# Performance work log

Hardware: AMD Instinct MI355X
Metric: run time of the kernel (lower is better)

Reference implementation:

```python
import jax, jax.numpy as jnp
import numpy as np

N_NODES = 80000
N_EDGES = 1280000
IN_CH = 128
HID = 64
N_GRAPHS = 64
DROPOUT_P = 0.3


def setup_inputs() -> dict:
    key = jax.random.key(0)
    ks = jax.random.split(key, 12)
    x = jax.random.normal(ks[0], (N_NODES, IN_CH), dtype=jnp.float32)
    edge_index = jax.random.randint(ks[1], (2, N_EDGES), 0, N_NODES, dtype=jnp.int64 if jax.config.read('jax_enable_x64') else jnp.int32)
    batch = jnp.sort(jax.random.randint(ks[2], (N_NODES,), 0, N_GRAPHS))
    def lin(k, fan_in, fan_out):
        lim = 1.0 / np.sqrt(fan_in)
        kw, kb = jax.random.split(k)
        W = jax.random.uniform(kw, (fan_in, fan_out), minval=-lim, maxval=lim, dtype=jnp.float32)
        b = jax.random.uniform(kb, (fan_out,), minval=-lim, maxval=lim, dtype=jnp.float32)
        return W, b
    W1, b1 = lin(ks[3], IN_CH, HID)
    W2, b2 = lin(ks[4], HID, HID)
    W3, b3 = lin(ks[5], HID, HID)
    Wm1, bm1 = lin(ks[6], HID, HID)
    Wm2, bm2 = lin(ks[7], HID, 1)
    return {"x": x, "edge_index": edge_index, "batch": batch,
            "W1": W1, "b1": b1, "W2": W2, "b2": b2, "W3": W3, "b3": b3,
            "Wm1": Wm1, "bm1": bm1, "Wm2": Wm2, "bm2": bm2}


def _gcn_conv(x, W, b, src, dst, deg_inv_sqrt):
    # PyG GCNConv: h = X W; add self-loops; norm_e = d^-1/2[src] * d^-1/2[dst]
    h = x @ W  # [N, F]
    norm = deg_inv_sqrt[src] * deg_inv_sqrt[dst]  # [E]
    agg = jax.ops.segment_sum(h[src] * norm[:, None], dst, num_segments=x.shape[0])
    agg = agg + h * (deg_inv_sqrt * deg_inv_sqrt)[:, None]  # self-loop term d^-1
    return agg + b


def _dropout(x, key, p):
    keep = jax.random.bernoulli(key, 1.0 - p, x.shape)
    return jnp.where(keep, x / (1.0 - p), 0.0)


def reference(x, edge_index, batch, W1, b1, W2, b2, W3, b3, Wm1, bm1, Wm2, bm2):
    src, dst = edge_index[0], edge_index[1]
    N = x.shape[0]
    # in-degree on dst, +1 for self-loop (PyG default normalization)
    deg = jax.ops.segment_sum(jnp.ones_like(dst, dtype=x.dtype), dst, num_segments=N) + 1.0
    deg_inv_sqrt = jax.lax.rsqrt(deg)

    dk = jax.random.split(jax.random.key(42), 4)
    h = _dropout(jax.nn.relu(_gcn_conv(x, W1, b1, src, dst, deg_inv_sqrt)), dk[0], DROPOUT_P)
    h = _dropout(jax.nn.relu(_gcn_conv(h, W2, b2, src, dst, deg_inv_sqrt)), dk[1], DROPOUT_P)
    h = _dropout(jax.nn.relu(_gcn_conv(h, W3, b3, src, dst, deg_inv_sqrt)), dk[2], DROPOUT_P)

    # global mean pool per graph
    sums = jax.ops.segment_sum(h, batch, num_segments=N_GRAPHS)
    counts = jax.ops.segment_sum(jnp.ones((N,), dtype=h.dtype), batch, num_segments=N_GRAPHS)
    pooled = sums / jnp.maximum(counts, 1.0)[:, None]  # [G, HID]

    # MLP head: Linear -> ReLU -> Dropout -> Linear
    m = jax.nn.relu(pooled @ Wm1 + bm1)
    m = _dropout(m, dk[3], DROPOUT_P)
    return m @ Wm2 + bm2  # [G, 1]
```

## Files before the change

kernel.cpp:

```cpp
#include <hip/hip_runtime.h>
#include <hip/hip_fp8.h>
#include <stdint.h>

#define HID 64
#define INCH 128
#define NGRAPH 64
#define KEEPP 0.7f
#define CAP 64
#define CAPSH 6
#define BD 16

typedef __attribute__((ext_vector_type(8))) short short8;
typedef __attribute__((ext_vector_type(4))) float floatx4;

__device__ __forceinline__ uint8_t f2e4(float f) {
  __hip_fp8_e4m3 t(f);
  return (uint8_t)t.__x;
}
__device__ __forceinline__ float e42f(uint8_t b) {
  __hip_fp8_e4m3 t;
  t.__x = (__hip_fp8_storage_t)b;
  return (float)t;
}
__device__ __forceinline__ ushort f2bf(float v) {
  uint32_t u = __float_as_uint(v);
  return (ushort)((u + 0x7FFFu + ((u >> 16) & 1u)) >> 16);
}
__device__ __forceinline__ float bf2f(ushort b) {
  return __uint_as_float((uint32_t)b << 16);
}

__host__ __device__ inline void tf2x32(uint32_t k0, uint32_t k1,
                                       uint32_t& x0, uint32_t& x1) {
  const uint32_t ks2 = k0 ^ k1 ^ 0x1BD11BDAu;
#define ROTL32(v, d) (((v) << (d)) | ((v) >> (32 - (d))))
#define TF_RND(r) { x0 += x1; x1 = ROTL32(x1, r); x1 ^= x0; }
  x0 += k0; x1 += k1;
  TF_RND(13) TF_RND(15) TF_RND(26) TF_RND(6)
  x0 += k1;  x1 += ks2 + 1u;
  TF_RND(17) TF_RND(29) TF_RND(16) TF_RND(24)
  x0 += ks2; x1 += k0 + 2u;
  TF_RND(13) TF_RND(15) TF_RND(26) TF_RND(6)
  x0 += k0;  x1 += k1 + 3u;
  TF_RND(17) TF_RND(29) TF_RND(16) TF_RND(24)
  x0 += k1;  x1 += ks2 + 4u;
  TF_RND(13) TF_RND(15) TF_RND(26) TF_RND(6)
  x0 += ks2; x1 += k0 + 5u;
#undef TF_RND
#undef ROTL32
}

__device__ __forceinline__ bool keep_mask(uint32_t k0, uint32_t k1, uint32_t idx) {
  uint32_t x0 = 0u, x1 = idx;
  tf2x32(k0, k1, x0, x1);
  uint32_t bits = x0 ^ x1;
  float u = __uint_as_float((bits >> 9) | 0x3f800000u) - 1.0f;
  return u < KEEPP;
}

__device__ __forceinline__ void wsplit_one(const float* __restrict__ W,
                                           short8* __restrict__ Wh,
                                           short8* __restrict__ Wl, int i) {
  int lane = i & 63, f = i >> 6;
  int kc = f >> 2, ct = f & 3;
  int kbase = kc * 32 + ((lane >> 4) << 3);
  int n = ct * 16 + (lane & 15);
  short8 h, l;
#pragma unroll
  for (int j = 0; j < 8; ++j) {
    float w = W[(size_t)(kbase + j) * HID + n];
    uint32_t u = __float_as_uint(w);
    h[j] = (short)(u >> 16);
    float r = w - __uint_as_float(u & 0xFFFF0000u);
    l[j] = (short)(__float_as_uint(r) >> 16);
  }
  Wh[i] = h;
  Wl[i] = l;
}

__global__ __launch_bounds__(256) void k_w1(const float* __restrict__ W1,
                                            short8* __restrict__ Wh1,
                                            short8* __restrict__ Wl1) {
  wsplit_one(W1, Wh1, Wl1, blockIdx.x * 256 + (int)threadIdx.x);
}

template <int K>
__device__ __forceinline__ void mgemm_tile_f32(const float* __restrict__ A,
                                               const short8* __restrict__ Wh,
                                               const short8* __restrict__ Wl,
                                               ushort* __restrict__ C,
                                               int N, int tile) {
  constexpr int KC = K / 32;
  const int lane = threadIdx.x & 63;
  const int wv = threadIdx.x >> 6;
  const int m = lane & 15;
  const int q = lane >> 4;
  const int row0 = tile * 64 + wv * 16;
  if (row0 >= N) return;
  const int arow = min(row0 + m, N - 1);
  const float* __restrict__ ap = A + (size_t)arow * K + (q << 3);

  floatx4 acc[4];
#pragma unroll
  for (int ct = 0; ct < 4; ++ct) acc[ct] = (floatx4){0.f, 0.f, 0.f, 0.f};

#pragma unroll
  for (int kc = 0; kc < KC; ++kc) {
    const floatx4* apv = (const floatx4*)(ap + kc * 32);
    floatx4 x0 = apv[0];
    floatx4 x1 = apv[1];
    short8 ah, al;
#pragma unroll
    for (int j = 0; j < 4; ++j) {
      uint32_t u = __float_as_uint(x0[j]);
      ah[j] = (short)(u >> 16);
      float r = x0[j] - __uint_as_float(u & 0xFFFF0000u);
      al[j] = (short)(__float_as_uint(r) >> 16);
    }
#pragma unroll
    for (int j = 0; j < 4; ++j) {
      uint32_t u = __float_as_uint(x1[j]);
      ah[4 + j] = (short)(u >> 16);
      float r = x1[j] - __uint_as_float(u & 0xFFFF0000u);
      al[4 + j] = (short)(__float_as_uint(r) >> 16);
    }
#pragma unroll
    for (int ct = 0; ct < 4; ++ct) {
      short8 bh = Wh[(kc * 4 + ct) * 64 + lane];
      short8 bl = Wl[(kc * 4 + ct) * 64 + lane];
      acc[ct] = __builtin_amdgcn_mfma_f32_16x16x32_bf16(ah, bh, acc[ct], 0, 0, 0);
      acc[ct] = __builtin_amdgcn_mfma_f32_16x16x32_bf16(ah, bl, acc[ct], 0, 0, 0);
      acc[ct] = __builtin_amdgcn_mfma_f32_16x16x32_bf16(al, bh, acc[ct], 0, 0, 0);
    }
  }

  ushort* __restrict__ cp = C + (size_t)row0 * HID;
#pragma unroll
  for (int ct = 0; ct < 4; ++ct)
#pragma unroll
    for (int r = 0; r < 4; ++r) {
      int rr = (q << 2) + r;
      if (row0 + rr < N) cp[(size_t)rr * HID + ct * 16 + m] = f2bf(acc[ct][r]);
    }
}

template <int K>
__global__ __launch_bounds__(256) void k_build_gemm(
    const float* __restrict__ A, const short8* __restrict__ Wh,
    const short8* __restrict__ Wl, ushort* __restrict__ C, int N,
    const int* __restrict__ src, const int* __restrict__ dst,
    int* __restrict__ counts, int* __restrict__ cap,
    int E, int build_blocks, int gemm_blocks,
    const float* __restrict__ W2, short8* __restrict__ Wh2, short8* __restrict__ Wl2,
    const float* __restrict__ W3, short8* __restrict__ Wh3, short8* __restrict__ Wl3,
    const int* __restrict__ batch, int* __restrict__ gends) {
  const int TB = build_blocks + gemm_blocks;
  const int tid = (int)threadIdx.x;
  if ((int)blockIdx.x >= TB) {
    int xb = (int)blockIdx.x - TB;
    if (xb < 2) {
      wsplit_one(W2, Wh2, Wl2, xb * 256 + tid);
    } else if (xb < 4) {
      wsplit_one(W3, Wh3, Wl3, (xb - 2) * 256 + tid);
    } else {
      int bi = xb - 4;
      for (int i = bi * 256 + tid; i < N; i += BD * 256) {
        int g = batch[i];
        int gn = (i + 1 < N) ? batch[i + 1] : -1;
        if (g != gn) gends[g] = i + 1;
      }
    }
    return;
  }
  const long T = (long)TB;
  const long b = (long)blockIdx.x;
  const long gb = (b * gemm_blocks) / T;
  const bool is_g = (((b + 1) * gemm_blocks) / T) != gb;
  if (!is_g) {
    int bb = (int)(b - gb);
    int e = bb * 256 + tid;
    if (e < E) {
      int s = src[e], d = dst[e];
      int r = atomicAdd(&counts[d], 1);
      if (r < CAP) cap[(d << CAPSH) + r] = s;
    }
    return;
  }
  mgemm_tile_f32<K>(A, Wh, Wl, C, N, (int)gb);
}

template <int K>
__global__ __launch_bounds__(256) void k_mgemm_b(const ushort* __restrict__ A,
                                                 const short8* __restrict__ Wh,
                                                 const short8* __restrict__ Wl,
                                                 uint8_t* __restrict__ C,
                                                 const int* __restrict__ counts,
                                                 int N) {
  constexpr int KC = K / 32;
  const int lane = threadIdx.x & 63;
  const int wv = threadIdx.x >> 6;
  const int m = lane & 15;
  const int q = lane >> 4;
  const int row0 = (int)blockIdx.x * 64 + wv * 16;
  if (row0 >= N) return;
  const int arow = min(row0 + m, N - 1);
  const ushort* __restrict__ ap = A + (size_t)arow * K + (q << 3);

  floatx4 acc[4];
#pragma unroll
  for (int ct = 0; ct < 4; ++ct) acc[ct] = (floatx4){0.f, 0.f, 0.f, 0.f};

#pragma unroll
  for (int kc = 0; kc < KC; ++kc) {
    short8 ah = *(const short8*)(ap + kc * 32);
#pragma unroll
    for (int ct = 0; ct < 4; ++ct) {
      short8 bh = Wh[(kc * 4 + ct) * 64 + lane];
      short8 bl = Wl[(kc * 4 + ct) * 64 + lane];
      acc[ct] = __builtin_amdgcn_mfma_f32_16x16x32_bf16(ah, bh, acc[ct], 0, 0, 0);
      acc[ct] = __builtin_amdgcn_mfma_f32_16x16x32_bf16(ah, bl, acc[ct], 0, 0, 0);
    }
  }

  float dv[4];
#pragma unroll
  for (int r = 0; r < 4; ++r) {
    int gr = min(row0 + (q << 2) + r, N - 1);
    dv[r] = rsqrtf((float)counts[gr] + 1.0f);
  }
  uint8_t* __restrict__ cp = C + (size_t)row0 * HID;
#pragma unroll
  for (int ct = 0; ct < 4; ++ct)
#pragma unroll
    for (int r = 0; r < 4; ++r) {
      int rr = (q << 2) + r;
      if (row0 + rr < N) cp[(size_t)rr * HID + ct * 16 + m] = f2e4(acc[ct][r] * dv[r]);
    }
}

__global__ __launch_bounds__(256) void k_scale(const ushort* __restrict__ Bh,
                                               const int* __restrict__ counts,
                                               uint8_t* __restrict__ B0, int N) {
  int t = blockIdx.x * 256 + threadIdx.x;
  int total = N * (HID / 8);
  if (t >= total) return;
  int node = t >> 3;
  float dn = rsqrtf((float)counts[node] + 1.0f);
  const ushort* ip = Bh + (size_t)t * 8;
  ushort4 a = *(const ushort4*)ip;
  ushort4 b = *(const ushort4*)(ip + 4);
  uint8_t o[8];
  o[0] = f2e4(bf2f(a.x) * dn); o[1] = f2e4(bf2f(a.y) * dn);
  o[2] = f2e4(bf2f(a.z) * dn); o[3] = f2e4(bf2f(a.w) * dn);
  o[4] = f2e4(bf2f(b.x) * dn); o[5] = f2e4(bf2f(b.y) * dn);
  o[6] = f2e4(bf2f(b.z) * dn); o[7] = f2e4(bf2f(b.w) * dn);
  *(uint2*)(B0 + (size_t)t * 8) = *(uint2*)o;
}

__global__ __launch_bounds__(256) void k_gather_s(const uint8_t* __restrict__ tmp,
                                                  const int* __restrict__ counts,
                                                  const int* __restrict__ cap,
                                                  const float* __restrict__ bias,
                                                  ushort* __restrict__ outh, int N,
                                                  uint32_t k0, uint32_t k1) {
  const int node = blockIdx.x * 4 + (threadIdx.x >> 6);
  const int lane = threadIdx.x & 63;
  if (node >= N) return;
  const int degn = __builtin_amdgcn_readfirstlane(counts[node]);
  const int deg = min(degn, CAP);
  const int base = node << CAPSH;
  const int idx = node * HID + lane;
  const float selfv = e42f(tmp[idx]);
  const float blane = bias[lane];
  const int sub = lane >> 4;
  const int ch4 = (lane & 15) << 2;
  float a0 = 0.0f, a1 = 0.0f, a2 = 0.0f, a3 = 0.0f;
  for (int j = 0; j < deg; j += 8) {
    int4 ea = *(const int4*)&cap[base + j];
    int4 eb = *(const int4*)&cap[base + j + 4];
    int sa = (sub & 1) ? ea.y : ea.x;
    int ta = (sub & 1) ? ea.w : ea.z;
    sa = (sub & 2) ? ta : sa;
    int sb = (sub & 1) ? eb.y : eb.x;
    int tb = (sub & 1) ? eb.w : eb.z;
    sb = (sub & 2) ? tb : sb;
    uint32_t wa = 0u, wb = 0u;
    if (j + sub < deg)
      wa = *(const uint32_t*)(tmp + ((size_t)sa << 6) + ch4);
    if (j + 4 + sub < deg)
      wb = *(const uint32_t*)(tmp + ((size_t)sb << 6) + ch4);
    a0 += e42f((uint8_t)(wa & 255u));
    a1 += e42f((uint8_t)((wa >> 8) & 255u));
    a2 += e42f((uint8_t)((wa >> 16) & 255u));
    a3 += e42f((uint8_t)(wa >> 24));
    a0 += e42f((uint8_t)(wb & 255u));
    a1 += e42f((uint8_t)((wb >> 8) & 255u));
    a2 += e42f((uint8_t)((wb >> 16) & 255u));
    a3 += e42f((uint8_t)(wb >> 24));
  }
  a0 += __shfl_xor(a0, 16); a1 += __shfl_xor(a1, 16);
  a2 += __shfl_xor(a2, 16); a3 += __shfl_xor(a3, 16);
  a0 += __shfl_xor(a0, 32); a1 += __shfl_xor(a1, 32);
  a2 += __shfl_xor(a2, 32); a3 += __shfl_xor(a3, 32);
  const int srcl = lane >> 2;
  float t0 = __shfl(a0, srcl);
  float t1 = __shfl(a1, srcl);
  float t2 = __shfl(a2, srcl);
  float t3 = __shfl(a3, srcl);
  float u01 = (lane & 1) ? t1 : t0;
  float u23 = (lane & 1) ? t3 : t2;
  float acc = (lane & 2) ? u23 : u01;

  const float dn = rsqrtf((float)degn + 1.0f);
  float v = dn * (acc + selfv) + blane;
  v = fmaxf(v, 0.0f);
  v = keep_mask(k0, k1, (uint32_t)idx) ? v / KEEPP : 0.0f;
  outh[idx] = f2bf(v);
}

__global__ __launch_bounds__(256) void k_pool(const ushort* __restrict__ h,
                                              const int* __restrict__ batch,
                                              float* __restrict__ sums, int N) {
  __shared__ float ls[NGRAPH * HID];
  for (int i = threadIdx.x; i < NGRAPH * HID; i += 256) ls[i] = 0.0f;
  __syncthreads();
  const int lane = threadIdx.x & 63;
  const int wave = threadIdx.x >> 6;
  int per = (N + gridDim.x - 1) / gridDim.x;
  int beg = blockIdx.x * per;
  int end = min(N, beg + per);
  for (int i = beg + wave; i < end; i += 4) {
    int g = batch[i];
    atomicAdd(&ls[g * HID + lane], bf2f(h[(size_t)i * HID + lane]));
  }
  __syncthreads();
  for (int i = threadIdx.x; i < NGRAPH * HID; i += 256)
    if (ls[i] != 0.0f) atomicAdd(&sums[i], ls[i]);
}

__global__ __launch_bounds__(256) void k_head(const float* __restrict__ sums,
                                              const int* __restrict__ gends,
                                              const float* __restrict__ Wm1,
                                              const float* __restrict__ bm1,
                                              const float* __restrict__ Wm2,
                                              const float* __restrict__ bm2,
                                              float* __restrict__ out,
                                              uint32_t k0, uint32_t k1) {
  __shared__ float cnts_s[NGRAPH];
  __shared__ float pooled[NGRAPH * HID];
  __shared__ float m[NGRAPH * HID];
  if (threadIdx.x < 64) {
    int g = threadIdx.x;
    int e = gends[g];
#pragma unroll
    for (int off = 1; off < 64; off <<= 1) {
      int o = __shfl_up(e, off);
      if (g >= off) e = max(e, o);
    }
    int prev = __shfl_up(e, 1);
    if (g == 0) prev = 0;
    cnts_s[g] = (float)(e - prev);
  }
  __syncthreads();
  for (int i = threadIdx.x; i < NGRAPH * HID; i += 256) {
    int g = i >> 6;
    pooled[i] = sums[i] / fmaxf(cnts_s[g], 1.0f);
  }
  __syncthreads();
  for (int i = threadIdx.x; i < NGRAPH * HID; i += 256) {
    int g = i >> 6, j = i & 63;
    float acc = bm1[j];
#pragma unroll 8
    for (int k = 0; k < HID; ++k)
      acc = fmaf(pooled[g * HID + k], Wm1[k * HID + j], acc);
    acc = fmaxf(acc, 0.0f);
    m[i] = keep_mask(k0, k1, (uint32_t)i) ? acc / KEEPP : 0.0f;
  }
  __syncthreads();
  if (threadIdx.x < NGRAPH) {
    int g = threadIdx.x;
    float acc = bm2[0];
#pragma unroll 8
    for (int j = 0; j < HID; ++j)
      acc = fmaf(m[g * HID + j], Wm2[j], acc);
    out[g] = acc;
  }
}

extern "C" void kernel_launch(void* const* d_in, const int* in_sizes, int n_in,
                              void* d_out, int out_size, void* d_ws, size_t ws_size,
                              hipStream_t stream) {
  const float* x     = (const float*)d_in[0];
  const int*   ei    = (const int*)d_in[1];
  const int*   batch = (const int*)d_in[2];
  const float* W1 = (const float*)d_in[3];
  const float* b1 = (const float*)d_in[4];
  const float* W2 = (const float*)d_in[5];
  const float* b2 = (const float*)d_in[6];
  const float* W3 = (const float*)d_in[7];
  const float* b3 = (const float*)d_in[8];
  const float* Wm1 = (const float*)d_in[9];
  const float* bm1 = (const float*)d_in[10];
  const float* Wm2 = (const float*)d_in[11];
  const float* bm2 = (const float*)d_in[12];
  float* out = (float*)d_out;

  const int N = in_sizes[0] / INCH;
  const int E = in_sizes[1] / 2;
  const int* src = ei;
  const int* dst = ei + E;

  char* ws = (char*)d_ws;
  size_t off = 0;
  uint8_t* B0 = (uint8_t*)(ws + off); off += (size_t)N * HID;
  off = (off + 15) & ~(size_t)15;
  ushort* B1    = (ushort*)(ws + off); off += (size_t)N * HID * 2;
  int*   counts = (int*)  (ws + off); off += (size_t)N * 4;
  float* sums   = (float*)(ws + off); off += NGRAPH * HID * 4;
  int*   gends  = (int*)  (ws + off); off += NGRAPH * 4;
  int*   cap    = (int*)  (ws + off); off += (size_t)N * CAP * 4;
  off = (off + 15) & ~(size_t)15;
  short8* Wh1 = (short8*)(ws + off); off += 1024 * 16;
  short8* Wl1 = (short8*)(ws + off); off += 1024 * 16;
  short8* Wh2 = (short8*)(ws + off); off += 512 * 16;
  short8* Wl2 = (short8*)(ws + off); off += 512 * 16;
  short8* Wh3 = (short8*)(ws + off); off += 512 * 16;
  short8* Wl3 = (short8*)(ws + off); off += 512 * 16;
  ushort* Bh = B1;

  uint32_t dk[4][2];
  for (uint32_t i = 0; i < 4; ++i) {
    uint32_t a = 0u, b = i;
    tf2x32(0u, 42u, a, b);
    dk[i][0] = a; dk[i][1] = b;
  }

  const int build_grid = (E + 255) / 256;
  const int mg_grid    = (N + 63) / 64;
  const int gath_grid  = (N + 3) / 4;
  const int scale_grid = (N * (HID / 8) + 255) / 256;

  hipMemsetAsync(counts, 0, (size_t)N * 4 + NGRAPH * HID * 4 + NGRAPH * 4, stream);
  k_w1<<<4, 256, 0, stream>>>(W1, Wh1, Wl1);

  k_build_gemm<INCH><<<build_grid + mg_grid + 4 + BD, 256, 0, stream>>>(
      x, Wh1, Wl1, Bh, N, src, dst, counts, cap, E,
      build_grid, mg_grid, W2, Wh2, Wl2, W3, Wh3, Wl3, batch, gends);
  k_scale<<<scale_grid, 256, 0, stream>>>(Bh, counts, B0, N);
  k_gather_s<<<gath_grid, 256, 0, stream>>>(B0, counts, cap, b1,
                                            B1, N, dk[0][0], dk[0][1]);
  k_mgemm_b<HID><<<mg_grid, 256, 0, stream>>>(B1, Wh2, Wl2, B0, counts, N);
  k_gather_s<<<gath_grid, 256, 0, stream>>>(B0, counts, cap, b2,
                                            B1, N, dk[1][0], dk[1][1]);
  k_mgemm_b<HID><<<mg_grid, 256, 0, stream>>>(B1, Wh3, Wl3, B0, counts, N);
  k_gather_s<<<gath_grid, 256, 0, stream>>>(B0, counts, cap, b3,
                                            B1, N, dk[2][0], dk[2][1]);

  k_pool<<<256, 256, 0, stream>>>(B1, batch, sums, N);
  k_head<<<1, 256, 0, stream>>>(sums, gends, Wm1, bm1, Wm2, bm2, out,
                                dk[3][0], dk[3][1]);
  (void)n_in; (void)out_size; (void)ws_size;
}
```

Before: 370.0 us.

## Fuse gather with next-layer GEMM and gather with mean pooling

Each aggregation pass now runs in the same kernel as the following layer's MFMA GEMM. A block gathers 64 nodes into a shared-memory bf16 tile, then multiplies that tile by the next weight matrix, so the bf16 hidden buffer no longer makes a global round trip. The final gather is fused with the per-graph pooling, which removes the last hidden-state write and read. The cost is fewer, larger blocks in the fused kernel: each wave processes 16 nodes serially, which reduces parallelism for latency-bound gathers. A second fp8 buffer is added so the kernel reads one buffer and writes the other.

New measurement: 373.1 us. About the same (+0.8%).

```diff
diff --git a/kernel.cpp b/kernel.cpp
--- a/kernel.cpp
+++ b/kernel.cpp
@@ -82,6 +82,60 @@
                                             short8* __restrict__ Wh1,
                                             short8* __restrict__ Wl1) {
   wsplit_one(W1, Wh1, Wl1, blockIdx.x * 256 + (int)threadIdx.x);
+}
+
+__device__ __forceinline__ float gather_node(const uint8_t* __restrict__ tmp,
+                                             const int* __restrict__ counts,
+                                             const int* __restrict__ cap,
+                                             int node, int lane, float blane,
+                                             uint32_t k0, uint32_t k1) {
+  const int degn = __builtin_amdgcn_readfirstlane(counts[node]);
+  const int deg = min(degn, CAP);
+  const int base = node << CAPSH;
+  const int idx = node * HID + lane;
+  const float selfv = e42f(tmp[idx]);
+  const int sub = lane >> 4;
+  const int ch4 = (lane & 15) << 2;
+  float a0 = 0.0f, a1 = 0.0f, a2 = 0.0f, a3 = 0.0f;
+  for (int j = 0; j < deg; j += 8) {
+    int4 ea = *(const int4*)&cap[base + j];
+    int4 eb = *(const int4*)&cap[base + j + 4];
+    int sa = (sub & 1) ? ea.y : ea.x;
+    int ta = (sub & 1) ? ea.w : ea.z;
+    sa = (sub & 2) ? ta : sa;
+    int sb = (sub & 1) ? eb.y : eb.x;
+    int tb = (sub & 1) ? eb.w : eb.z;
+    sb = (sub & 2) ? tb : sb;
+    uint32_t wa = 0u, wb = 0u;
+    if (j + sub < deg)
+      wa = *(const uint32_t*)(tmp + ((size_t)sa << 6) + ch4);
+    if (j + 4 + sub < deg)
+      wb = *(const uint32_t*)(tmp + ((size_t)sb << 6) + ch4);
+    a0 += e42f((uint8_t)(wa & 255u));
+    a1 += e42f((uint8_t)((wa >> 8) & 255u));
+    a2 += e42f((uint8_t)((wa >> 16) & 255u));
+    a3 += e42f((uint8_t)(wa >> 24));
+    a0 += e42f((uint8_t)(wb & 255u));
+    a1 += e42f((uint8_t)((wb >> 8) & 255u));
+    a2 += e42f((uint8_t)((wb >> 16) & 255u));
+    a3 += e42f((uint8_t)(wb >> 24));
+  }
+  a0 += __shfl_xor(a0, 16); a1 += __shfl_xor(a1, 16);
+  a2 += __shfl_xor(a2, 16); a3 += __shfl_xor(a3, 16);
+  a0 += __shfl_xor(a0, 32); a1 += __shfl_xor(a1, 32);
+  a2 += __shfl_xor(a2, 32); a3 += __shfl_xor(a3, 32);
+  const int srcl = lane >> 2;
+  float t0 = __shfl(a0, srcl);
+  float t1 = __shfl(a1, srcl);
+  float t2 = __shfl(a2, srcl);
+  float t3 = __shfl(a3, srcl);
+  float u01 = (lane & 1) ? t1 : t0;
+  float u23 = (lane & 1) ? t3 : t2;
+  float acc = (lane & 2) ? u23 : u01;
+  const float dn = rsqrtf((float)degn + 1.0f);
+  float v = dn * (acc + selfv) + blane;
+  v = fmaxf(v, 0.0f);
+  return keep_mask(k0, k1, (uint32_t)idx) ? v / KEEPP : 0.0f;
 }
 
 template <int K>
@@ -189,55 +243,6 @@
   mgemm_tile_f32<K>(A, Wh, Wl, C, N, (int)gb);
 }
 
-template <int K>
-__global__ __launch_bounds__(256) void k_mgemm_b(const ushort* __restrict__ A,
-                                                 const short8* __restrict__ Wh,
-                                                 const short8* __restrict__ Wl,
-                                                 uint8_t* __restrict__ C,
-                                                 const int* __restrict__ counts,
-                                                 int N) {
-  constexpr int KC = K / 32;
-  const int lane = threadIdx.x & 63;
-  const int wv = threadIdx.x >> 6;
-  const int m = lane & 15;
-  const int q = lane >> 4;
-  const int row0 = (int)blockIdx.x * 64 + wv * 16;
-  if (row0 >= N) return;
-  const int arow = min(row0 + m, N - 1);
-  const ushort* __restrict__ ap = A + (size_t)arow * K + (q << 3);
-
-  floatx4 acc[4];
-#pragma unroll
-  for (int ct = 0; ct < 4; ++ct) acc[ct] = (floatx4){0.f, 0.f, 0.f, 0.f};
-
-#pragma unroll
-  for (int kc = 0; kc < KC; ++kc) {
-    short8 ah = *(const short8*)(ap + kc * 32);
-#pragma unroll
-    for (int ct = 0; ct < 4; ++ct) {
-      short8 bh = Wh[(kc * 4 + ct) * 64 + lane];
-      short8 bl = Wl[(kc * 4 + ct) * 64 + lane];
-      acc[ct] = __builtin_amdgcn_mfma_f32_16x16x32_bf16(ah, bh, acc[ct], 0, 0, 0);
-      acc[ct] = __builtin_amdgcn_mfma_f32_16x16x32_bf16(ah, bl, acc[ct], 0, 0, 0);
-    }
-  }
-
-  float dv[4];
-#pragma unroll
-  for (int r = 0; r < 4; ++r) {
-    int gr = min(row0 + (q << 2) + r, N - 1);
-    dv[r] = rsqrtf((float)counts[gr] + 1.0f);
-  }
-  uint8_t* __restrict__ cp = C + (size_t)row0 * HID;
-#pragma unroll
-  for (int ct = 0; ct < 4; ++ct)
-#pragma unroll
-    for (int r = 0; r < 4; ++r) {
-      int rr = (q << 2) + r;
-      if (row0 + rr < N) cp[(size_t)rr * HID + ct * 16 + m] = f2e4(acc[ct][r] * dv[r]);
-    }
-}
-
 __global__ __launch_bounds__(256) void k_scale(const ushort* __restrict__ Bh,
                                                const int* __restrict__ counts,
                                                uint8_t* __restrict__ B0, int N) {
@@ -257,81 +262,84 @@
   *(uint2*)(B0 + (size_t)t * 8) = *(uint2*)o;
 }
 
-__global__ __launch_bounds__(256) void k_gather_s(const uint8_t* __restrict__ tmp,
-                                                  const int* __restrict__ counts,
-                                                  const int* __restrict__ cap,
-                                                  const float* __restrict__ bias,
-                                                  ushort* __restrict__ outh, int N,
-                                                  uint32_t k0, uint32_t k1) {
-  const int node = blockIdx.x * 4 + (threadIdx.x >> 6);
+__global__ __launch_bounds__(256) void k_fused(const uint8_t* __restrict__ tmp,
+                                               const int* __restrict__ counts,
+                                               const int* __restrict__ cap,
+                                               const float* __restrict__ bias,
+                                               const short8* __restrict__ Wh,
+                                               const short8* __restrict__ Wl,
+                                               uint8_t* __restrict__ Cout, int N,
+                                               uint32_t k0, uint32_t k1) {
+  __shared__ ushort hs[64][72];
   const int lane = threadIdx.x & 63;
-  if (node >= N) return;
-  const int degn = __builtin_amdgcn_readfirstlane(counts[node]);
-  const int deg = min(degn, CAP);
-  const int base = node << CAPSH;
-  const int idx = node * HID + lane;
-  const float selfv = e42f(tmp[idx]);
+  const int wv = threadIdx.x >> 6;
+  const int node0 = (int)blockIdx.x * 64;
   const float blane = bias[lane];
-  const int sub = lane >> 4;
-  const int ch4 = (lane & 15) << 2;
-  float a0 = 0.0f, a1 = 0.0f, a2 = 0.0f, a3 = 0.0f;
-  for (int j = 0; j < deg; j += 8) {
-    int4 ea = *(const int4*)&cap[base + j];
-    int4 eb = *(const int4*)&cap[base + j + 4];
-    int sa = (sub & 1) ? ea.y : ea.x;
-    int ta = (sub & 1) ? ea.w : ea.z;
-    sa = (sub & 2) ? ta : sa;
-    int sb = (sub & 1) ? eb.y : eb.x;
-    int tb = (sub & 1) ? eb.w : eb.z;
-    sb = (sub & 2) ? tb : sb;
-    uint32_t wa = 0u, wb = 0u;
-    if (j + sub < deg)
-      wa = *(const uint32_t*)(tmp + ((size_t)sa << 6) + ch4);
-    if (j + 4 + sub < deg)
-      wb = *(const uint32_t*)(tmp + ((size_t)sb << 6) + ch4);
-    a0 += e42f((uint8_t)(wa & 255u));
-    a1 += e42f((uint8_t)((wa >> 8) & 255u));
-    a2 += e42f((uint8_t)((wa >> 16) & 255u));
-    a3 += e42f((uint8_t)(wa >> 24));
-    a0 += e42f((uint8_t)(wb & 255u));
-    a1 += e42f((uint8_t)((wb >> 8) & 255u));
-    a2 += e42f((uint8_t)((wb >> 16) & 255u));
-    a3 += e42f((uint8_t)(wb >> 24));
-  }
-  a0 += __shfl_xor(a0, 16); a1 += __shfl_xor(a1, 16);
-  a2 += __shfl_xor(a2, 16); a3 += __shfl_xor(a3, 16);
-  a0 += __shfl_xor(a0, 32); a1 += __shfl_xor(a1, 32);
-  a2 += __shfl_xor(a2, 32); a3 += __shfl_xor(a3, 32);
-  const int srcl = lane >> 2;
-  float t0 = __shfl(a0, srcl);
-  float t1 = __shfl(a1, srcl);
-  float t2 = __shfl(a2, srcl);
-  float t3 = __shfl(a3, srcl);
-  float u01 = (lane & 1) ? t1 : t0;
-  float u23 = (lane & 1) ? t3 : t2;
-  float acc = (lane & 2) ? u23 : u01;
-
-  const float dn = rsqrtf((float)degn + 1.0f);
-  float v = dn * (acc + selfv) + blane;
-  v = fmaxf(v, 0.0f);
-  v = keep_mask(k0, k1, (uint32_t)idx) ? v / KEEPP : 0.0f;
-  outh[idx] = f2bf(v);
-}
-
-__global__ __launch_bounds__(256) void k_pool(const ushort* __restrict__ h,
-                                              const int* __restrict__ batch,
-                                              float* __restrict__ sums, int N) {
+
+  for (int i = 0; i < 16; ++i) {
+    const int node = node0 + wv * 16 + i;
+    float v = 0.0f;
+    if (node < N)
+      v = gather_node(tmp, counts, cap, node, lane, blane, k0, k1);
+    hs[wv * 16 + i][lane] = f2bf(v);
+  }
+
+  const int m = lane & 15;
+  const int q = lane >> 4;
+  const int row0 = node0 + wv * 16;
+  if (row0 >= N) return;
+
+  floatx4 acc[4];
+#pragma unroll
+  for (int ct = 0; ct < 4; ++ct) acc[ct] = (floatx4){0.f, 0.f, 0.f, 0.f};
+#pragma unroll
+  for (int kc = 0; kc < 2; ++kc) {
+    short8 ah = *(const short8*)&hs[wv * 16 + m][kc * 32 + q * 8];
+#pragma unroll
+    for (int ct = 0; ct < 4; ++ct) {
+      short8 bh = Wh[(kc * 4 + ct) * 64 + lane];
+      short8 bl = Wl[(kc * 4 + ct) * 64 + lane];
+      acc[ct] = __builtin_amdgcn_mfma_f32_16x16x32_bf16(ah, bh, acc[ct], 0, 0, 0);
+      acc[ct] = __builtin_amdgcn_mfma_f32_16x16x32_bf16(ah, bl, acc[ct], 0, 0, 0);
+    }
+  }
+
+  float dv[4];
+#pragma unroll
+  for (int r = 0; r < 4; ++r) {
+    int gr = min(row0 + (q << 2) + r, N - 1);
+    dv[r] = rsqrtf((float)counts[gr] + 1.0f);
+  }
+  uint8_t* __restrict__ cp = Cout + (size_t)row0 * HID;
+#pragma unroll
+  for (int ct = 0; ct < 4; ++ct)
+#pragma unroll
+    for (int r = 0; r < 4; ++r) {
+      int rr = (q << 2) + r;
+      if (row0 + rr < N) cp[(size_t)rr * HID + ct * 16 + m] = f2e4(acc[ct][r] * dv[r]);
+    }
+}
+
+__global__ __launch_bounds__(256) void k_gather_pool(const uint8_t* __restrict__ tmp,
+                                                     const int* __restrict__ counts,
+                                                     const int* __restrict__ cap,
+                                                     const float* __restrict__ bias,
+                                                     const int* __restrict__ batch,
+                                                     float* __restrict__ sums, int N,
+                                                     uint32_t k0, uint32_t k1) {
   __shared__ float ls[NGRAPH * HID];
   for (int i = threadIdx.x; i < NGRAPH * HID; i += 256) ls[i] = 0.0f;
   __syncthreads();
   const int lane = threadIdx.x & 63;
-  const int wave = threadIdx.x >> 6;
+  const int wv = threadIdx.x >> 6;
+  const float blane = bias[lane];
   int per = (N + gridDim.x - 1) / gridDim.x;
   int beg = blockIdx.x * per;
   int end = min(N, beg + per);
-  for (int i = beg + wave; i < end; i += 4) {
-    int g = batch[i];
-    atomicAdd(&ls[g * HID + lane], bf2f(h[(size_t)i * HID + lane]));
+  for (int node = beg + wv; node < end; node += 4) {
+    float v = gather_node(tmp, counts, cap, node, lane, blane, k0, k1);
+    int g = __builtin_amdgcn_readfirstlane(batch[node]);
+    atomicAdd(&ls[g * HID + lane], v);
   }
   __syncthreads();
   for (int i = threadIdx.x; i < NGRAPH * HID; i += 256)
@@ -412,9 +420,12 @@
 
   char* ws = (char*)d_ws;
   size_t off = 0;
-  uint8_t* B0 = (uint8_t*)(ws + off); off += (size_t)N * HID;
-  off = (off + 15) & ~(size_t)15;
-  ushort* B1    = (ushort*)(ws + off); off += (size_t)N * HID * 2;
+  uint8_t* B0  = (uint8_t*)(ws + off); off += (size_t)N * HID;
+  off = (off + 63) & ~(size_t)63;
+  uint8_t* B0b = (uint8_t*)(ws + off); off += (size_t)N * HID;
+  off = (off + 63) & ~(size_t)63;
+  ushort* Bh    = (ushort*)(ws + off); off += (size_t)N * HID * 2;
+  off = (off + 63) & ~(size_t)63;
   int*   counts = (int*)  (ws + off); off += (size_t)N * 4;
   float* sums   = (float*)(ws + off); off += NGRAPH * HID * 4;
   int*   gends  = (int*)  (ws + off); off += NGRAPH * 4;
@@ -426,7 +437,6 @@
   short8* Wl2 = (short8*)(ws + off); off += 512 * 16;
   short8* Wh3 = (short8*)(ws + off); off += 512 * 16;
   short8* Wl3 = (short8*)(ws + off); off += 512 * 16;
-  ushort* Bh = B1;
 
   uint32_t dk[4][2];
   for (uint32_t i = 0; i < 4; ++i) {
@@ -437,7 +447,6 @@
 
   const int build_grid = (E + 255) / 256;
   const int mg_grid    = (N + 63) / 64;
-  const int gath_grid  = (N + 3) / 4;
   const int scale_grid = (N * (HID / 8) + 255) / 256;
 
   hipMemsetAsync(counts, 0, (size_t)N * 4 + NGRAPH * HID * 4 + NGRAPH * 4, stream);
@@ -447,16 +456,14 @@
       x, Wh1, Wl1, Bh, N, src, dst, counts, cap, E,
       build_grid, mg_grid, W2, Wh2, Wl2, W3, Wh3, Wl3, batch, gends);
   k_scale<<<scale_grid, 256, 0, stream>>>(Bh, counts, B0, N);
-  k_gather_s<<<gath_grid, 256, 0, stream>>>(B0, counts, cap, b1,
-                                            B1, N, dk[0][0], dk[0][1]);
-  k_mgemm_b<HID><<<mg_grid, 256, 0, stream>>>(B1, Wh2, Wl2, B0, counts, N);
-  k_gather_s<<<gath_grid, 256, 0, stream>>>(B0, counts, cap, b2,
-                                            B1, N, dk[1][0], dk[1][1]);
-  k_mgemm_b<HID><<<mg_grid, 256, 0, stream>>>(B1, Wh3, Wl3, B0, counts, N);
-  k_gather_s<<<gath_grid, 256, 0, stream>>>(B0, counts, cap, b3,
-                                            B1, N, dk[2][0], dk[2][1]);
-
-  k_pool<<<256, 256, 0, stream>>>(B1, batch, sums, N);
+
+  k_fused<<<mg_grid, 256, 0, stream>>>(B0, counts, cap, b1, Wh2, Wl2,
+                                       B0b, N, dk[0][0], dk[0][1]);
+  k_fused<<<mg_grid, 256, 0, stream>>>(B0b, counts, cap, b2, Wh3, Wl3,
+                                       B0, N, dk[1][0], dk[1][1]);
+
+  k_gather_pool<<<1024, 256, 0, stream>>>(B0, counts, cap, b3, batch, sums,
+                                          N, dk[2][0], dk[2][1]);
   k_head<<<1, 256, 0, stream>>>(sums, gends, Wm1, bm1, Wm2, bm2, out,
                                 dk[3][0], dk[3][1]);
   (void)n_in; (void)out_size; (void)ws_size;
```
